# Kernel optimization log

Hardware: AMD Instinct MI355X
Metric: run time of the kernel (lower is better)

## Reference

```python
import jax, jax.numpy as jnp
import numpy as np

AGENT_TYPE_VEHICLE = 1
AGENT_TYPE_PEDESTRIAN = 2
N_VEHICLE_INTENTIONS = 6
N_PEDESTRIAN_INTENTIONS = 2
INTENTION_LOGIT_DIM = 6


def setup_inputs() -> dict:
    key = jax.random.key(0)
    ks = jax.random.split(key, 10)
    B, N, D = 32, 2048, 512
    H = D // 2
    s_in = 1.0 / np.sqrt(D)
    s_h = 1.0 / np.sqrt(H)
    return {
        "repr3": jax.random.normal(ks[0], (B, N, D), dtype=jnp.float32),
        "agent_type_ids": jax.random.randint(ks[1], (B, N), 0, 4, dtype=jnp.int64),
        # vehicle head: Linear(D, D//2) -> GELU -> Linear(D//2, 6)
        "vW1": jax.random.normal(ks[2], (H, D), dtype=jnp.float32) * s_in,
        "vb1": jax.random.normal(ks[3], (H,), dtype=jnp.float32) * s_in,
        "vW2": jax.random.normal(ks[4], (N_VEHICLE_INTENTIONS, H), dtype=jnp.float32) * s_h,
        "vb2": jax.random.normal(ks[5], (N_VEHICLE_INTENTIONS,), dtype=jnp.float32) * s_h,
        # pedestrian head: Linear(D, D//2) -> GELU -> Linear(D//2, 2)
        "pW1": jax.random.normal(ks[6], (H, D), dtype=jnp.float32) * s_in,
        "pb1": jax.random.normal(ks[7], (H,), dtype=jnp.float32) * s_in,
        "pW2": jax.random.normal(ks[8], (N_PEDESTRIAN_INTENTIONS, H), dtype=jnp.float32) * s_h,
        "pb2": jax.random.normal(ks[9], (N_PEDESTRIAN_INTENTIONS,), dtype=jnp.float32) * s_h,
    }


def _mlp(x, W1, b1, W2, b2):
    # x: [B,N,D] -> [B,N,out]; exact (erf) GELU matches torch nn.GELU()
    h = jax.nn.gelu(jnp.einsum("bnd,hd->bnh", x, W1) + b1, approximate=False)
    return jnp.einsum("bnh,oh->bno", h, W2) + b2


def reference(repr3, agent_type_ids, vW1, vb1, vW2, vb2, pW1, pb1, pW2, pb2):
    v_mask = agent_type_ids == AGENT_TYPE_VEHICLE  # [B,N]
    p_mask = agent_type_ids == AGENT_TYPE_PEDESTRIAN
    v_logits = _mlp(repr3, vW1, vb1, vW2, vb2)  # [B,N,6]
    p_logits = _mlp(repr3, pW1, pb1, pW2, pb2)  # [B,N,2]
    pad = INTENTION_LOGIT_DIM - N_PEDESTRIAN_INTENTIONS
    p_padded = jnp.pad(p_logits, ((0, 0), (0, 0), (0, pad)))  # [B,N,6]
    zero = jnp.zeros((), dtype=repr3.dtype)
    intention_logits = (
        jnp.where(v_mask[..., None], v_logits, zero)
        + jnp.where(p_mask[..., None], p_padded, zero)
    )
    return intention_logits, v_mask, p_mask
```

## Files before the change

### kernel.cpp

```cpp
#include <hip/hip_runtime.h>
#include <hip/hip_bf16.h>
#include <math.h>


#define TOKENS 65536
#define DIM    512
#define HID    256
#define ASTR   40
#define HSTR   264

using short8 = __attribute__((ext_vector_type(8))) short;
using f32x4  = __attribute__((ext_vector_type(4))) float;

#define BAR()                                                      \
    do {                                                           \
        __builtin_amdgcn_sched_barrier(0);                         \
        asm volatile("s_waitcnt lgkmcnt(0)" ::: "memory");         \
        __builtin_amdgcn_s_barrier();                              \
        __builtin_amdgcn_sched_barrier(0);                         \
    } while (0)

__device__ __forceinline__ unsigned int pkrne(float a, float b) {
    unsigned int ua = __float_as_uint(a);
    unsigned int ub = __float_as_uint(b);
    ua += 0x7FFFu + ((ua >> 16) & 1u);
    ub += 0x7FFFu + ((ub >> 16) & 1u);
    return __builtin_amdgcn_perm(ub, ua, 0x07060302u);
}

__device__ __forceinline__ uint2 cvt4(f32x4 v) {
    return make_uint2(pkrne(v[0], v[1]), pkrne(v[2], v[3]));
}

__device__ __forceinline__ __hip_bfloat16 bf16rne(float x) {
    unsigned int u = __float_as_uint(x);
    u += 0x7FFFu + ((u >> 16) & 1u);
    unsigned short hs = (unsigned short)(u >> 16);
    return *(__hip_bfloat16*)&hs;
}

__device__ __forceinline__ float gelu_exact(float x) {
    const float z  = fabsf(x) * 0.7071067811865475f;
    const float t  = __builtin_amdgcn_rcpf(fmaf(0.3275911f, z, 1.0f));
    float p = fmaf(1.061405429f, t, -1.453152027f);
    p = fmaf(p, t, 1.421413741f);
    p = fmaf(p, t, -0.284496736f);
    p = fmaf(p, t, 0.254829592f);
    p = p * t;
    const float e  = __expf(-z * z);
    const float er = fmaf(-p, e, 1.0f);
    return 0.5f * x * (1.0f + copysignf(er, x));
}

__global__ __launch_bounds__(256)
void prep_kernel(const float* __restrict__ vW1, const float* __restrict__ pW1,
                 const float* __restrict__ vW2, const float* __restrict__ pW2,
                 __hip_bfloat16* __restrict__ Wc, __hip_bfloat16* __restrict__ W2c)
{
    const int i = blockIdx.x * 256 + threadIdx.x;
    if (i < 32768) {
        const int lane = i & 63;
        const int it   = (i >> 6) & 15;
        const int nt   = i >> 10;
        const int head = nt >> 4;
        const int row  = (nt & 15) * 16 + (lane & 15);
        const int k    = it * 32 + (lane >> 4) * 8;
        const float* src = (head ? pW1 : vW1) + row * DIM + k;
        f32x4 a = *(const f32x4*)(src);
        f32x4 b = *(const f32x4*)(src + 4);
        uint2 lo = cvt4(a), hi = cvt4(b);
        *(uint4*)((char*)Wc + (long)i * 16) = make_uint4(lo.x, lo.y, hi.x, hi.y);
    } else if (i < 32768 + 1024) {
        const int c    = i - 32768;
        const int lane = c & 63;
        const int rest = c >> 6;
        const int head = rest & 1;
        const int ks   = rest >> 1;
        const int l16  = lane & 15;
        const int quad = lane >> 4;
        const int nOut = head ? 2 : 6;
        uint4 o = make_uint4(0u, 0u, 0u, 0u);
        if (l16 < nOut) {
            const float* src = (head ? pW2 : vW2) + l16 * HID + ks * 32 + quad * 8;
            f32x4 a = *(const f32x4*)(src);
            f32x4 b = *(const f32x4*)(src + 4);
            uint2 lo = cvt4(a), hi = cvt4(b);
            o = make_uint4(lo.x, lo.y, hi.x, hi.y);
        }
        *(uint4*)((char*)W2c + (long)c * 16) = o;
    }
}

__global__ __launch_bounds__(512, 6)
void intention_heads_kernel(const float* __restrict__ X,
                            const int* __restrict__ ids,
                            const __hip_bfloat16* __restrict__ Wc,
                            const __hip_bfloat16* __restrict__ W2c,
                            const float* __restrict__ vb1,
                            const float* __restrict__ pb1,
                            const float* __restrict__ vb2,
                            const float* __restrict__ pb2,
                            float* __restrict__ out)
{
    __shared__ __align__(16) unsigned char smem[64 * HSTR * 2];
    __hip_bfloat16* H = (__hip_bfloat16*)smem;

    const int cpx = gridDim.x >> 3;
    const int bid = (blockIdx.x & 7) * cpx + (blockIdx.x >> 3);

    const int head = bid & 1;
    const int row0 = (bid >> 1) * 64;

    const int tid  = threadIdx.x;
    const int wave = tid >> 6;
    const int lane = tid & 63;
    const int quad = lane >> 4;
    const int l16  = lane & 15;
    const int wcol = wave * 32;

    const int q = tid & 7;
    const int r = tid >> 3;
    const float* Xs = X + (long)(row0 + r) * DIM + q * 4;

    const char* Bq = (const char*)Wc
                   + (long)(head * 16 + wave * 2) * 16384 + (long)lane * 16;

    f32x4 acc[4][2];
    #pragma unroll
    for (int i = 0; i < 4; ++i)
        #pragma unroll
        for (int j = 0; j < 2; ++j)
            acc[i][j] = (f32x4){0.f, 0.f, 0.f, 0.f};

    f32x4 ga = *(const f32x4*)(Xs);
    {
        __hip_bfloat16* A = (__hip_bfloat16*)smem;
        *(uint2*)&A[r * ASTR + q * 4] = cvt4(ga);
    }
    BAR();

    #pragma unroll
    for (int it = 0; it < DIM / 32; ++it) {
        __hip_bfloat16* cur = (__hip_bfloat16*)(smem + (it & 1) * 5120);
        __hip_bfloat16* nxt = (__hip_bfloat16*)(smem + ((it + 1) & 1) * 5120);

        if (it < 15)
            ga = *(const f32x4*)(Xs + (it + 1) * 32);

        short8 bc[2];
        #pragma unroll
        for (int j = 0; j < 2; ++j)
            bc[j] = *(const short8*)(Bq + j * 16384 + it * 1024);

        short8 af[4];
        #pragma unroll
        for (int i = 0; i < 4; ++i)
            af[i] = *(const short8*)&cur[(i * 16 + l16) * ASTR + quad * 8];

        #pragma unroll
        for (int i = 0; i < 4; ++i)
            #pragma unroll
            for (int j = 0; j < 2; ++j)
                acc[i][j] = __builtin_amdgcn_mfma_f32_16x16x32_bf16(af[i], bc[j], acc[i][j], 0, 0, 0);

        if (it < 15)
            *(uint2*)&nxt[r * ASTR + q * 4] = cvt4(ga);
        BAR();
    }

    const float* b1 = head ? pb1 : vb1;
    float b1v[2];
    #pragma unroll
    for (int j = 0; j < 2; ++j)
        b1v[j] = b1[wcol + j * 16 + l16];

    #pragma unroll
    for (int i = 0; i < 4; ++i) {
        #pragma unroll
        for (int j = 0; j < 2; ++j) {
            const int col = wcol + j * 16 + l16;
            #pragma unroll
            for (int rr = 0; rr < 4; ++rr) {
                const int row = i * 16 + quad * 4 + rr;
                H[row * HSTR + col] = bf16rne(gelu_exact(acc[i][j][rr] + b1v[j]));
            }
        }
    }
    BAR();

    if (wave < 4) {
        const float* b2 = head ? pb2 : vb2;
        const int nOut = head ? 2 : 6;

        f32x4 acc2 = (f32x4){0.f, 0.f, 0.f, 0.f};
        const int tokb = wave * 16;
        const short* hbase = (const short*)&H[(tokb + l16) * HSTR + quad * 8];
        const char*  w2q   = (const char*)W2c + head * 1024 + (long)lane * 16;
        #pragma unroll
        for (int ks = 0; ks < 8; ++ks) {
            short8 af    = *(const short8*)(hbase + ks * 32);
            short8 bfrag = *(const short8*)(w2q + ks * 2048);
            acc2 = __builtin_amdgcn_mfma_f32_16x16x32_bf16(af, bfrag, acc2, 0, 0, 0);
        }

        const float b2v = (l16 < nOut) ? b2[l16] : 0.0f;

        #pragma unroll
        for (int rr = 0; rr < 4; ++rr) {
            const int t = row0 + tokb + quad * 4 + rr;
            const int type = ids[t];
            if (head == 0) {
                if (l16 == 0) {
                    out[TOKENS * 6 + t] = (type == 1) ? 1.0f : 0.0f;
                    out[TOKENS * 7 + t] = (type == 2) ? 1.0f : 0.0f;
                }
                if (l16 < 6) {
                    if (type == 1)
                        out[t * 6 + l16] = acc2[rr] + b2v;
                    else if (type != 2)
                        out[t * 6 + l16] = 0.0f;
                }
            } else {
                if (l16 < 6 && type == 2)
                    out[t * 6 + l16] = (l16 < 2) ? (acc2[rr] + b2v) : 0.0f;
            }
        }
    }
}

extern "C" void kernel_launch(void* const* d_in, const int* in_sizes, int n_in,
                              void* d_out, int out_size, void* d_ws, size_t ws_size,
                              hipStream_t stream) {
    (void)n_in; (void)out_size; (void)ws_size;
    const float* X   = (const float*)d_in[0];
    const int*   ids = (const int*)d_in[1];
    const float* vW1 = (const float*)d_in[2];
    const float* vb1 = (const float*)d_in[3];
    const float* vW2 = (const float*)d_in[4];
    const float* vb2 = (const float*)d_in[5];
    const float* pW1 = (const float*)d_in[6];
    const float* pb1 = (const float*)d_in[7];
    const float* pW2 = (const float*)d_in[8];
    const float* pb2 = (const float*)d_in[9];
    float* out = (float*)d_out;

    __hip_bfloat16* Wc  = (__hip_bfloat16*)d_ws;
    __hip_bfloat16* W2c = Wc + 512 * DIM;

    hipLaunchKernelGGL(prep_kernel, dim3(132), dim3(256), 0, stream,
                       vW1, pW1, vW2, pW2, Wc, W2c);

    const int tokens = in_sizes[1];
    const int grid   = (tokens / 64) * 2;

    hipLaunchKernelGGL(intention_heads_kernel, dim3(grid), dim3(512), 0, stream,
                       X, ids, Wc, W2c, vb1, pb1, vb2, pb2, out);
}
```

Before: 253.9 us.

## Compact vehicle and pedestrian token indices to skip masked MLP work

Adds a compaction kernel that writes the masks, zeroes the logits and builds index lists of vehicle and pedestrian tokens using wave-ballot atomics. The main kernel then runs each head only on gathered tiles of matching tokens and exits early past the count, so roughly half of the GEMM work and X reads are avoided. In exchange it adds an extra launch, a gathered (non-contiguous) row load of X, and scattered output writes; ordering from the atomics is nondeterministic but results are unaffected.

After: 287.3 us. +13.2%, slower.

```diff
diff --git a/kernel.cpp b/kernel.cpp
--- a/kernel.cpp
+++ b/kernel.cpp
@@ -55,9 +55,11 @@
 __global__ __launch_bounds__(256)
 void prep_kernel(const float* __restrict__ vW1, const float* __restrict__ pW1,
                  const float* __restrict__ vW2, const float* __restrict__ pW2,
-                 __hip_bfloat16* __restrict__ Wc, __hip_bfloat16* __restrict__ W2c)
+                 __hip_bfloat16* __restrict__ Wc, __hip_bfloat16* __restrict__ W2c,
+                 int* __restrict__ cnt)
 {
     const int i = blockIdx.x * 256 + threadIdx.x;
+    if (i < 2) cnt[i] = 0;
     if (i < 32768) {
         const int lane = i & 63;
         const int it   = (i >> 6) & 15;
@@ -91,9 +93,49 @@
     }
 }
 
+__global__ __launch_bounds__(256)
+void compact_kernel(const int* __restrict__ ids, float* __restrict__ out,
+                    int* __restrict__ cnt,
+                    int* __restrict__ idxV, int* __restrict__ idxP)
+{
+    const int i = blockIdx.x * 256 + threadIdx.x;
+    const int type = ids[i];
+    out[TOKENS * 6 + i] = (type == 1) ? 1.0f : 0.0f;
+    out[TOKENS * 7 + i] = (type == 2) ? 1.0f : 0.0f;
+    uint2 z = make_uint2(0u, 0u);
+    uint2* p = (uint2*)(out + (long)i * 6);
+    p[0] = z; p[1] = z; p[2] = z;
+
+    const int lane = threadIdx.x & 63;
+    const unsigned long long below = (lane == 63) ? ~0ull >> 1
+                                   : (1ull << lane) - 1ull;
+    {
+        unsigned long long m = __ballot(type == 1);
+        if (m) {
+            const int leader = __ffsll((long long)m) - 1;
+            int base = 0;
+            if (lane == leader) base = atomicAdd(cnt + 0, __popcll(m));
+            base = __shfl(base, leader);
+            if (type == 1) idxV[base + __popcll(m & below)] = i;
+        }
+    }
+    {
+        unsigned long long m = __ballot(type == 2);
+        if (m) {
+            const int leader = __ffsll((long long)m) - 1;
+            int base = 0;
+            if (lane == leader) base = atomicAdd(cnt + 1, __popcll(m));
+            base = __shfl(base, leader);
+            if (type == 2) idxP[base + __popcll(m & below)] = i;
+        }
+    }
+}
+
 __global__ __launch_bounds__(512, 6)
 void intention_heads_kernel(const float* __restrict__ X,
-                            const int* __restrict__ ids,
+                            const int* __restrict__ cnt,
+                            const int* __restrict__ idxV,
+                            const int* __restrict__ idxP,
                             const __hip_bfloat16* __restrict__ Wc,
                             const __hip_bfloat16* __restrict__ W2c,
                             const float* __restrict__ vb1,
@@ -109,7 +151,11 @@
     const int bid = (blockIdx.x & 7) * cpx + (blockIdx.x >> 3);
 
     const int head = bid & 1;
-    const int row0 = (bid >> 1) * 64;
+    const int tile = bid >> 1;
+    const int count = cnt[head];
+    if (tile * 64 >= count) return;
+    const int* __restrict__ idx = head ? idxP : idxV;
+    const int base = tile * 64;
 
     const int tid  = threadIdx.x;
     const int wave = tid >> 6;
@@ -120,7 +166,9 @@
 
     const int q = tid & 7;
     const int r = tid >> 3;
-    const float* Xs = X + (long)(row0 + r) * DIM + q * 4;
+    const int slot  = base + r;
+    const int tok   = idx[(slot < count) ? slot : (count - 1)];
+    const float* Xs = X + (long)tok * DIM + q * 4;
 
     const char* Bq = (const char*)Wc
                    + (long)(head * 16 + wave * 2) * 16384 + (long)lane * 16;
@@ -207,22 +255,10 @@
 
         #pragma unroll
         for (int rr = 0; rr < 4; ++rr) {
-            const int t = row0 + tokb + quad * 4 + rr;
-            const int type = ids[t];
-            if (head == 0) {
-                if (l16 == 0) {
-                    out[TOKENS * 6 + t] = (type == 1) ? 1.0f : 0.0f;
-                    out[TOKENS * 7 + t] = (type == 2) ? 1.0f : 0.0f;
-                }
-                if (l16 < 6) {
-                    if (type == 1)
-                        out[t * 6 + l16] = acc2[rr] + b2v;
-                    else if (type != 2)
-                        out[t * 6 + l16] = 0.0f;
-                }
-            } else {
-                if (l16 < 6 && type == 2)
-                    out[t * 6 + l16] = (l16 < 2) ? (acc2[rr] + b2v) : 0.0f;
+            const int s = base + tokb + quad * 4 + rr;
+            if (s < count && l16 < nOut) {
+                const int t = idx[s];
+                out[t * 6 + l16] = acc2[rr] + b2v;
             }
         }
     }
@@ -244,15 +280,19 @@
     const float* pb2 = (const float*)d_in[9];
     float* out = (float*)d_out;
 
-    __hip_bfloat16* Wc  = (__hip_bfloat16*)d_ws;
-    __hip_bfloat16* W2c = Wc + 512 * DIM;
+    char* ws = (char*)d_ws;
+    __hip_bfloat16* Wc  = (__hip_bfloat16*)ws;
+    __hip_bfloat16* W2c = (__hip_bfloat16*)(ws + 512 * 1024);
+    int* cnt  = (int*)(ws + 512 * 1024 + 16 * 1024);
+    int* idxV = (int*)(ws + 512 * 1024 + 16 * 1024 + 256);
+    int* idxP = idxV + TOKENS;
 
     hipLaunchKernelGGL(prep_kernel, dim3(132), dim3(256), 0, stream,
-                       vW1, pW1, vW2, pW2, Wc, W2c);
-
-    const int tokens = in_sizes[1];
-    const int grid   = (tokens / 64) * 2;
-
-    hipLaunchKernelGGL(intention_heads_kernel, dim3(grid), dim3(512), 0, stream,
-                       X, ids, Wc, W2c, vb1, pb1, vb2, pb2, out);
-}
+                       vW1, pW1, vW2, pW2, Wc, W2c, cnt);
+
+    hipLaunchKernelGGL(compact_kernel, dim3(TOKENS / 256), dim3(256), 0, stream,
+                       ids, out, cnt, idxV, idxP);
+
+    hipLaunchKernelGGL(intention_heads_kernel, dim3(2048), dim3(512), 0, stream,
+                       X, cnt, idxV, idxP, Wc, W2c, vb1, pb1, vb2, pb2, out);
+}
```
